# Performance work log

Hardware: AMD Instinct MI355X
Metric: run time of the kernel (lower is better)

The kernel has to match this reference:

```python
import jax, jax.numpy as jnp
import numpy as np

D_IN = 2048
D_LATENT = 16384
BATCH = 4096
K = 64


def setup_inputs() -> dict:
    key = jax.random.key(0)
    k1, k2, k3 = jax.random.split(key, 3)
    s_enc = 1.0 / np.sqrt(D_IN)
    s_dec = 1.0 / np.sqrt(D_LATENT)
    return {
        "x": jax.random.normal(k1, (BATCH, D_IN), dtype=jnp.float32),
        "W_enc": jax.random.normal(k2, (D_LATENT, D_IN), dtype=jnp.float32) * s_enc,
        "b_enc": jnp.zeros((D_LATENT,), dtype=jnp.float32),
        "W_dec": jax.random.normal(k3, (D_IN, D_LATENT), dtype=jnp.float32) * s_dec,
        "b_dec": jnp.zeros((D_IN,), dtype=jnp.float32),
        "k": K,
    }


def reference(x, W_enc, b_enc, W_dec, b_dec, k):
    # encode: dense GEMM + ReLU  -> h: [B, d_latent]
    h = jax.nn.relu(jnp.einsum("bd,ld->bl", x, W_enc) + b_enc)
    # top-k masking over latent dim (dim=1)
    _, idx = jax.lax.top_k(h, k)  # idx: [B, k]
    B = h.shape[0]
    mask = jnp.zeros(h.shape, dtype=bool).at[jnp.arange(B)[:, None], idx].set(True)
    h_topk = jnp.where(mask, h, jnp.zeros((), dtype=h.dtype))
    # decode: GEMM through sparse latents
    x_hat = jnp.einsum("bl,dl->bd", h_topk, W_dec) + b_dec
    return x_hat, h, h_topk
```

## Files before the change

### kernel.cpp

```cpp
#include <hip/hip_runtime.h>
#include <cstdint>

#define DIN   2048
#define DLAT  16384
#define NB    4096
#define KSEL  64
#define MAXC  128
#define CAP   2048
#define TAU   1.5f

typedef unsigned short u16;
typedef unsigned int   u32;
typedef __attribute__((ext_vector_type(8))) short short8;
typedef __attribute__((ext_vector_type(4))) float f32x4;
typedef __attribute__((ext_vector_type(4))) u32  u32x4;

#define GLOAD_LDS16(g, l)                                              \
    __builtin_amdgcn_global_load_lds(                                  \
        (const __attribute__((address_space(1))) void*)(g),            \
        (__attribute__((address_space(3))) void*)(l), 16, 0, 0)

__device__ __forceinline__ u32 f32_to_bf16(u32 u)
{
    u += 0x7FFFu + ((u >> 16) & 1u);
    return u >> 16;
}

__device__ __forceinline__ float bf16_to_f32(u16 w)
{
    return __uint_as_float((u32)w << 16);
}

__global__ __launch_bounds__(256)
void zero_cnt_kernel(u32* __restrict__ cnt)
{
    const int i = blockIdx.x * 256 + threadIdx.x;
    if (i < NB) cnt[i] = 0u;
}

__global__ __launch_bounds__(256)
void cvt_f32_bf16_kernel(const float* __restrict__ in, u16* __restrict__ out, int n8)
{
    const int i = blockIdx.x * 256 + threadIdx.x;
    if (i >= n8) return;
    const float4* p = reinterpret_cast<const float4*>(in) + (size_t)i * 2;
    const float4 a = p[0], b = p[1];
    const float v[8] = {a.x, a.y, a.z, a.w, b.x, b.y, b.z, b.w};
    u32 r[8];
#pragma unroll
    for (int j = 0; j < 8; ++j) r[j] = f32_to_bf16(__float_as_uint(v[j]));
    uint4 o;
    o.x = r[0] | (r[1] << 16);
    o.y = r[2] | (r[3] << 16);
    o.z = r[4] | (r[5] << 16);
    o.w = r[6] | (r[7] << 16);
    reinterpret_cast<uint4*>(out)[i] = o;
}

template <bool APPEND>
__global__ __launch_bounds__(512, 2)
void sae_encode_8ph(const u16* __restrict__ XB, const u16* __restrict__ WB,
                    const float* __restrict__ benc, float* __restrict__ H,
                    u32* __restrict__ cnt, uint2* __restrict__ cand)
{
    __shared__ __align__(16) u16 lds[65536];

    const int tid = threadIdx.x;
    const int wv  = tid >> 6;
    const int ln  = tid & 63;
    const int wm  = wv >> 2;
    const int wn  = wv & 3;
    const int fr  = ln & 15;
    const int fq  = ln >> 4;

    const int b   = blockIdx.x;
    const int wg  = (b & 7) * 128 + (b >> 3);
    const int m_blk = wg & 15;
    const int n_blk = wg >> 4;
    const size_t bm = (size_t)m_blk * 256;
    const size_t bn = (size_t)n_blk * 256;

    const int sslot = (ln & 3) ^ ((ln >> 3) & 3);
    const int srow  = wv * 16 + (ln >> 2);
    const u16* aSrc = XB + (bm + srow) * (size_t)DIN + sslot * 8;
    const u16* bSrc = WB + (bn + srow) * (size_t)DIN + sslot * 8;
    const size_t rowStep = (size_t)128 * DIN;

    auto STG = [&](int mat, int tile, int kkh) {
        const u16* s0 = (mat ? bSrc : aSrc) + tile * 64 + kkh * 32;
        const int dst = (tile & 1) * 32768 + mat * 16384 + kkh * 8192 + wv * 512;
        GLOAD_LDS16(s0,           &lds[dst]);
        GLOAD_LDS16(s0 + rowStep, &lds[dst + 4096]);
    };

    f32x4 acc[8][4];
#pragma unroll
    for (int i = 0; i < 8; ++i)
#pragma unroll
        for (int j = 0; j < 4; ++j) acc[i][j] = (f32x4)0.0f;

    const int swb = (fq ^ ((fr >> 1) & 3)) * 8;
    const int arow0 = wm * 128 + fr;
    const int brow0 = wn * 64 + fr;

    STG(0, 0, 0); STG(1, 0, 0);
    STG(0, 0, 1); STG(1, 0, 1);
    STG(0, 1, 0); STG(1, 1, 0);

    short8 aR[8], bX[2], bY[2];

    for (int g = 0; g < 32; ++g) {
        const int buf = (g & 1) * 32768;

        if (g < 31) asm volatile("s_waitcnt vmcnt(8)" ::: "memory");
        else        asm volatile("s_waitcnt vmcnt(4)" ::: "memory");
        __builtin_amdgcn_s_barrier();
#pragma unroll
        for (int mi = 0; mi < 8; ++mi)
            aR[mi] = *reinterpret_cast<const short8*>(
                &lds[buf + (arow0 + mi * 16) * 32 + swb]);
        bX[0] = *reinterpret_cast<const short8*>(&lds[buf + 16384 + (brow0 +  0) * 32 + swb]);
        bX[1] = *reinterpret_cast<const short8*>(&lds[buf + 16384 + (brow0 + 16) * 32 + swb]);
        if (g < 31) { STG(0, g + 1, 1); STG(1, g + 1, 1); }
        asm volatile("s_waitcnt lgkmcnt(0)" ::: "memory");
        __builtin_amdgcn_sched_barrier(0);
        __builtin_amdgcn_s_setprio(1);
#pragma unroll
        for (int mi = 0; mi < 8; ++mi) {
            acc[mi][0] = __builtin_amdgcn_mfma_f32_16x16x32_bf16(aR[mi], bX[0], acc[mi][0], 0, 0, 0);
            acc[mi][1] = __builtin_amdgcn_mfma_f32_16x16x32_bf16(aR[mi], bX[1], acc[mi][1], 0, 0, 0);
        }
        __builtin_amdgcn_s_setprio(0);

        __builtin_amdgcn_s_barrier();
        bY[0] = *reinterpret_cast<const short8*>(&lds[buf + 16384 + (brow0 + 32) * 32 + swb]);
        bY[1] = *reinterpret_cast<const short8*>(&lds[buf + 16384 + (brow0 + 48) * 32 + swb]);
        if (g < 30) STG(0, g + 2, 0);
        asm volatile("s_waitcnt lgkmcnt(0)" ::: "memory");
        __builtin_amdgcn_sched_barrier(0);
        __builtin_amdgcn_s_setprio(1);
#pragma unroll
        for (int mi = 0; mi < 8; ++mi) {
            acc[mi][2] = __builtin_amdgcn_mfma_f32_16x16x32_bf16(aR[mi], bY[0], acc[mi][2], 0, 0, 0);
            acc[mi][3] = __builtin_amdgcn_mfma_f32_16x16x32_bf16(aR[mi], bY[1], acc[mi][3], 0, 0, 0);
        }
        __builtin_amdgcn_s_setprio(0);

        if (g < 30)       asm volatile("s_waitcnt vmcnt(10)" ::: "memory");
        else if (g == 30) asm volatile("s_waitcnt vmcnt(8)"  ::: "memory");
        else              asm volatile("s_waitcnt vmcnt(0)"  ::: "memory");
        __builtin_amdgcn_s_barrier();
#pragma unroll
        for (int mi = 0; mi < 8; ++mi)
            aR[mi] = *reinterpret_cast<const short8*>(
                &lds[buf + 8192 + (arow0 + mi * 16) * 32 + swb]);
        bY[0] = *reinterpret_cast<const short8*>(&lds[buf + 24576 + (brow0 + 32) * 32 + swb]);
        bY[1] = *reinterpret_cast<const short8*>(&lds[buf + 24576 + (brow0 + 48) * 32 + swb]);
        if (g < 30) STG(1, g + 2, 0);
        asm volatile("s_waitcnt lgkmcnt(0)" ::: "memory");
        __builtin_amdgcn_sched_barrier(0);
        __builtin_amdgcn_s_setprio(1);
#pragma unroll
        for (int mi = 0; mi < 8; ++mi) {
            acc[mi][2] = __builtin_amdgcn_mfma_f32_16x16x32_bf16(aR[mi], bY[0], acc[mi][2], 0, 0, 0);
            acc[mi][3] = __builtin_amdgcn_mfma_f32_16x16x32_bf16(aR[mi], bY[1], acc[mi][3], 0, 0, 0);
        }
        __builtin_amdgcn_s_setprio(0);

        bX[0] = *reinterpret_cast<const short8*>(&lds[buf + 24576 + (brow0 +  0) * 32 + swb]);
        bX[1] = *reinterpret_cast<const short8*>(&lds[buf + 24576 + (brow0 + 16) * 32 + swb]);
        asm volatile("s_waitcnt lgkmcnt(0)" ::: "memory");
        __builtin_amdgcn_sched_barrier(0);
        __builtin_amdgcn_s_setprio(1);
#pragma unroll
        for (int mi = 0; mi < 8; ++mi) {
            acc[mi][0] = __builtin_amdgcn_mfma_f32_16x16x32_bf16(aR[mi], bX[0], acc[mi][0], 0, 0, 0);
            acc[mi][1] = __builtin_amdgcn_mfma_f32_16x16x32_bf16(aR[mi], bX[1], acc[mi][1], 0, 0, 0);
        }
        __builtin_amdgcn_s_setprio(0);
    }

#pragma unroll
    for (int ni = 0; ni < 4; ++ni) {
        const size_t col = bn + wn * 64 + ni * 16 + fr;
        const float be = benc[col];
#pragma unroll
        for (int mi = 0; mi < 8; ++mi) {
            const size_t r0 = bm + wm * 128 + mi * 16 + fq * 4;
            const f32x4 v = acc[mi][ni];
#pragma unroll
            for (int j = 0; j < 4; ++j) {
                const float val = fmaxf(v[j] + be, 0.0f);
                __builtin_nontemporal_store(val, &H[(r0 + j) * DLAT + col]);
                if (APPEND && val > TAU) {
                    const u32 p = atomicAdd(&cnt[r0 + j], 1u);
                    if (p < CAP)
                        cand[(r0 + j) * (size_t)CAP + p] =
                            make_uint2((u32)col, __float_as_uint(val));
                }
            }
        }
    }
}

__global__ __launch_bounds__(256, 4)
void sae_encode_kernel(const float* __restrict__ X, const float* __restrict__ W,
                       const float* __restrict__ benc, float* __restrict__ H)
{
    __shared__ float As[32][132];
    __shared__ float Bs[32][132];

    const int tid  = threadIdx.x;
    const int bm   = blockIdx.y * 128;
    const int bn   = blockIdx.x * 128;

    const int wave = tid >> 6;
    const int lane = tid & 63;
    const int tm   = ((wave >> 1) << 3) + (lane >> 3);
    const int tn   = ((wave &  1) << 3) + (lane &  7);

    float acc[8][8];
#pragma unroll
    for (int i = 0; i < 8; ++i)
#pragma unroll
        for (int j = 0; j < 8; ++j) acc[i][j] = 0.0f;

    const int lrow = tid >> 1;
    const int lcol = (tid & 1) << 4;

    const float* xptr = X + (size_t)(bm + lrow) * DIN + lcol;
    const float* wptr = W + (size_t)(bn + lrow) * DIN + lcol;

    for (int k0 = 0; k0 < DIN; k0 += 32) {
#pragma unroll
        for (int i = 0; i < 4; ++i) {
            const float4 av = *reinterpret_cast<const float4*>(xptr + k0 + 4 * i);
            const float4 bv = *reinterpret_cast<const float4*>(wptr + k0 + 4 * i);
            const int kk = lcol + 4 * i;
            As[kk + 0][lrow] = av.x; As[kk + 1][lrow] = av.y;
            As[kk + 2][lrow] = av.z; As[kk + 3][lrow] = av.w;
            Bs[kk + 0][lrow] = bv.x; Bs[kk + 1][lrow] = bv.y;
            Bs[kk + 2][lrow] = bv.z; Bs[kk + 3][lrow] = bv.w;
        }
        __syncthreads();

#pragma unroll 8
        for (int k = 0; k < 32; ++k) {
            const float4 a0 = *reinterpret_cast<const float4*>(&As[k][tm * 8]);
            const float4 a1 = *reinterpret_cast<const float4*>(&As[k][tm * 8 + 4]);
            const float4 b0 = *reinterpret_cast<const float4*>(&Bs[k][tn * 8]);
            const float4 b1 = *reinterpret_cast<const float4*>(&Bs[k][tn * 8 + 4]);
            const float a[8] = {a0.x, a0.y, a0.z, a0.w, a1.x, a1.y, a1.z, a1.w};
            const float b[8] = {b0.x, b0.y, b0.z, b0.w, b1.x, b1.y, b1.z, b1.w};
#pragma unroll
            for (int i = 0; i < 8; ++i)
#pragma unroll
                for (int j = 0; j < 8; ++j)
                    acc[i][j] = fmaf(a[i], b[j], acc[i][j]);
        }
        __syncthreads();
    }

#pragma unroll
    for (int i = 0; i < 8; ++i) {
        float* orow = H + (size_t)(bm + tm * 8 + i) * DLAT + bn + tn * 8;
#pragma unroll
        for (int j = 0; j < 8; j += 4) {
            float4 o;
            o.x = fmaxf(acc[i][j + 0] + benc[bn + tn * 8 + j + 0], 0.0f);
            o.y = fmaxf(acc[i][j + 1] + benc[bn + tn * 8 + j + 1], 0.0f);
            o.z = fmaxf(acc[i][j + 2] + benc[bn + tn * 8 + j + 2], 0.0f);
            o.w = fmaxf(acc[i][j + 3] + benc[bn + tn * 8 + j + 3], 0.0f);
            *reinterpret_cast<float4*>(orow + j) = o;
        }
    }
}

__device__ __forceinline__ int blk_scan256(int v, volatile int* wsum,
                                           int ln, int wv, int& total)
{
#pragma unroll
    for (int off = 1; off < 64; off <<= 1) {
        const int n = __shfl_up(v, off, 64);
        if (ln >= off) v += n;
    }
    if (ln == 63) wsum[wv] = v;
    __syncthreads();
    int add = 0;
#pragma unroll
    for (int c = 0; c < 3; ++c) if (c < wv) add += wsum[c];
    total = wsum[0] + wsum[1] + wsum[2] + wsum[3];
    __syncthreads();
    return v + add;
}

__device__ __forceinline__ void refine_np(const float* __restrict__ Wenc,
                                          const float* __restrict__ benc,
                                          const float* __restrict__ xs,
                                          int C, const int* cand_idx,
                                          float* cand_val, float psum[32][6],
                                          int tid)
{
    const int g = tid >> 3;
    const int p = tid & 7;
    for (int c0 = 0; c0 < C; c0 += 32) {
        const int ci = c0 + g;
        if (ci < C && p < 6) {
            const int li = cand_idx[ci];
            const float* __restrict__ wr = Wenc + (size_t)li * DIN;
            const int ks = (p < 4) ? p * 384 : 1536 + (p - 4) * 256;
            const int ke = ks + ((p < 4) ? 384 : 256);
            float s = 0.0f;
            for (int k = ks; k < ke; k += 32) {
                float4 w4[8];
#pragma unroll
                for (int j = 0; j < 8; ++j)
                    w4[j] = *reinterpret_cast<const float4*>(wr + k + 4 * j);
#pragma unroll
                for (int j = 0; j < 8; ++j) {
                    const float4 x4 = *reinterpret_cast<const float4*>(xs + k + 4 * j);
                    s = fmaf(x4.x, w4[j].x, s);
                    s = fmaf(x4.y, w4[j].y, s);
                    s = fmaf(x4.z, w4[j].z, s);
                    s = fmaf(x4.w, w4[j].w, s);
                }
            }
            psum[g][p] = s;
        }
        __syncthreads();
        if (ci < C && p == 0) {
            float total = 0.0f;
#pragma unroll
            for (int q = 0; q < 6; ++q)
                total = __fadd_rn(total, psum[g][q]);
            total = __fadd_rn(total, benc[cand_idx[ci]]);
            cand_val[ci] = fmaxf(total, 0.0f);
        }
        __syncthreads();
    }
}

__global__ __launch_bounds__(256)
void sae_topk_compact(const u32* __restrict__ cnt, const uint2* __restrict__ cand,
                      const float* __restrict__ X, const float* __restrict__ Wenc,
                      const float* __restrict__ benc, float* __restrict__ Ht,
                      float band, const u16* __restrict__ WT,
                      const float* __restrict__ bdec, float* __restrict__ xhat)
{
    __shared__ __align__(16) float xs[DIN];
    __shared__ u32  lidx[CAP];
    __shared__ u32  lval[CAP];
    __shared__ u32  hist[4][256];
    __shared__ int  scan_[256];
    __shared__ int  wsum[4];
    __shared__ int  sh_bin, sh_above;
    __shared__ int   cand_idx[MAXC];
    __shared__ float cand_val[MAXC];
    __shared__ unsigned char cand_sel[MAXC];
    __shared__ float psum[32][6];
    __shared__ int   sel_i[KSEL];
    __shared__ float sel_v[KSEL];
    __shared__ int   dec_i[KSEL];
    __shared__ float dec_v[KSEL];

    const int tid = threadIdx.x;
    const int wv  = tid >> 6;
    const int ln  = tid & 63;
    const int row = blockIdx.x;

    const int n = min((int)cnt[row], CAP);

    {
        const float4* xp = reinterpret_cast<const float4*>(X + (size_t)row * DIN);
        reinterpret_cast<float4*>(xs)[tid * 2 + 0] = xp[tid * 2 + 0];
        reinterpret_cast<float4*>(xs)[tid * 2 + 1] = xp[tid * 2 + 1];
    }
    if (tid < KSEL) { dec_i[tid] = 0; dec_v[tid] = 0.0f; }
    for (int i = tid; i < n; i += 256) {
        const uint2 e = cand[(size_t)row * CAP + i];
        lidx[i] = e.x;
        lval[i] = e.y;
    }
    __syncthreads();

    u32 prefix = 0, msk = 0;
    int kk = KSEL;
    for (int pass = 0; pass < 3; ++pass) {
        const int shift = 24 - 8 * pass;
        hist[0][tid] = 0; hist[1][tid] = 0; hist[2][tid] = 0; hist[3][tid] = 0;
        __syncthreads();
        for (int i = tid; i < n; i += 256) {
            const u32 x = lval[i];
            if ((x & msk) == prefix)
                atomicAdd(&hist[wv][(x >> shift) & 255u], 1u);
        }
        __syncthreads();
        int val = (int)(hist[0][255 - tid] + hist[1][255 - tid] +
                        hist[2][255 - tid] + hist[3][255 - tid]);
#pragma unroll
        for (int off = 1; off < 64; off <<= 1) {
            const int nn = __shfl_up(val, off, 64);
            if (ln >= off) val += nn;
        }
        if (ln == 63) wsum[wv] = val;
        __syncthreads();
        int add = 0;
#pragma unroll
        for (int c = 0; c < 3; ++c) if (c < wv) add += wsum[c];
        scan_[tid] = val + add;
        __syncthreads();
        {
            const int binh = (int)(hist[0][tid] + hist[1][tid] +
                                   hist[2][tid] + hist[3][tid]);
            const int ge = scan_[255 - tid];
            const int gt = ge - binh;
            if (gt < kk && ge >= kk) { sh_bin = tid; sh_above = gt; }
        }
        __syncthreads();
        prefix |= ((u32)sh_bin) << shift;
        msk    |= 0xFFu << shift;
        kk     -= sh_above;
        __syncthreads();
    }

    const float Tf = __uint_as_float(prefix);
    const float hi = Tf + band;
    const float lo = Tf - band;

    int c_safe = 0, c_band = 0;
    for (int i = tid; i < n; i += 256) {
        const float f = __uint_as_float(lval[i]);
        c_safe += (f > hi) ? 1 : 0;
        c_band += (f >= lo && f <= hi) ? 1 : 0;
    }
    int S;
    (void)blk_scan256(c_safe, wsum, ln, wv, S);
    int totC;
    const int bincl = blk_scan256(c_band, wsum, ln, wv, totC);
    int bpos = bincl - c_band;
    int C = totC;
    if (C > MAXC) C = MAXC;
    int need = KSEL - S;
    if (need > C) need = C;

    for (int i = tid; i < n; i += 256) {
        const float f = __uint_as_float(lval[i]);
        if (f >= lo && f <= hi) {
            if (bpos < MAXC) cand_idx[bpos] = (int)lidx[i];
            ++bpos;
        }
    }
    __syncthreads();

    refine_np(Wenc, benc, xs, C, cand_idx, cand_val, psum, tid);

    if (tid < C) {
        const float val = cand_val[tid];
        const int  myi = cand_idx[tid];
        int r = 0;
        for (int m = 0; m < C; ++m)
            r += (cand_val[m] > val ||
                  (cand_val[m] == val && cand_idx[m] < myi)) ? 1 : 0;
        cand_sel[tid] = (r < need) ? 1 : 0;
    }
    __syncthreads();

    int csel = 0;
    for (int i = tid; i < n; i += 256) {
        const float f = __uint_as_float(lval[i]);
        bool s = (f > hi);
        if (!s && f >= lo && f <= hi) {
            const int gi = (int)lidx[i];
            for (int m = 0; m < C; ++m)
                if (cand_idx[m] == gi) { s = (cand_sel[m] != 0); break; }
        }
        csel += s ? 1 : 0;
    }
    int totSel;
    int spos = blk_scan256(csel, wsum, ln, wv, totSel) - csel;
    if (totSel > KSEL) totSel = KSEL;
    for (int i = tid; i < n; i += 256) {
        const float f = __uint_as_float(lval[i]);
        bool s = (f > hi);
        if (!s && f >= lo && f <= hi) {
            const int gi = (int)lidx[i];
            for (int m = 0; m < C; ++m)
                if (cand_idx[m] == gi) { s = (cand_sel[m] != 0); break; }
        }
        if (s) {
            if (spos < KSEL) { sel_i[spos] = (int)lidx[i]; sel_v[spos] = f; }
            ++spos;
        }
    }
    __syncthreads();

    if (tid < totSel) {
        const int id = sel_i[tid];
        int r = 0;
        for (int m = 0; m < totSel; ++m)
            r += (sel_i[m] < id) ? 1 : 0;
        dec_i[r] = id;
        dec_v[r] = sel_v[tid];
    }
    __syncthreads();

    float* orow = Ht + (size_t)row * DLAT;
    {
        f32x4 z; z.x = 0.0f; z.y = 0.0f; z.z = 0.0f; z.w = 0.0f;
#pragma unroll
        for (int j = 0; j < 16; ++j)
            __builtin_nontemporal_store(z,
                reinterpret_cast<f32x4*>(orow + j * 1024 + tid * 4));
    }
    __syncthreads();
    if (tid < totSel) orow[dec_i[tid]] = dec_v[tid];

    const int d = tid * 8;
    float4 a0 = *reinterpret_cast<const float4*>(bdec + d);
    float4 a1 = *reinterpret_cast<const float4*>(bdec + d + 4);
#pragma unroll 8
    for (int j = 0; j < KSEL; ++j) {
        const float f = dec_v[j];
        const int   l = dec_i[j];
        const u16* wp = WT + (size_t)l * DIN + d;
        const ushort4 w0 = *reinterpret_cast<const ushort4*>(wp);
        const ushort4 w1 = *reinterpret_cast<const ushort4*>(wp + 4);
        a0.x = fmaf(f, bf16_to_f32(w0.x), a0.x);
        a0.y = fmaf(f, bf16_to_f32(w0.y), a0.y);
        a0.z = fmaf(f, bf16_to_f32(w0.z), a0.z);
        a0.w = fmaf(f, bf16_to_f32(w0.w), a0.w);
        a1.x = fmaf(f, bf16_to_f32(w1.x), a1.x);
        a1.y = fmaf(f, bf16_to_f32(w1.y), a1.y);
        a1.z = fmaf(f, bf16_to_f32(w1.z), a1.z);
        a1.w = fmaf(f, bf16_to_f32(w1.w), a1.w);
    }
    float* xo = xhat + (size_t)row * DIN + d;
    f32x4 s0; s0.x = a0.x; s0.y = a0.y; s0.z = a0.z; s0.w = a0.w;
    f32x4 s1; s1.x = a1.x; s1.y = a1.y; s1.z = a1.z; s1.w = a1.w;
    __builtin_nontemporal_store(s0, reinterpret_cast<f32x4*>(xo));
    __builtin_nontemporal_store(s1, reinterpret_cast<f32x4*>(xo + 4));
}

template <bool FUSE, bool WRITE_LISTS>
__global__ __launch_bounds__(256)
void sae_topk_kernel(const float* __restrict__ H, const float* __restrict__ X,
                     const float* __restrict__ Wenc, const float* __restrict__ benc,
                     float* __restrict__ Ht, int* __restrict__ sidx,
                     float* __restrict__ sval, float band,
                     const u16* __restrict__ WT, const float* __restrict__ bdec,
                     float* __restrict__ xhat)
{
    __shared__ __align__(16) float xs[DIN];
    __shared__ u32  hist[4][256];
    __shared__ int  scan_[256];
    __shared__ int  wsum[4];
    __shared__ int  sh_bin, sh_above;
    __shared__ int           cand_idx[MAXC];
    __shared__ float         cand_val[MAXC];
    __shared__ unsigned char cand_sel[MAXC];
    __shared__ float psum[32][6];
    __shared__ int   dec_idx[KSEL];
    __shared__ float dec_val[KSEL];

    const int tid = threadIdx.x;
    const int wv  = tid >> 6;
    const int ln  = tid & 63;
    const int row = blockIdx.x;
    const u32* __restrict__ hrow =
        reinterpret_cast<const u32*>(H) + (size_t)row * DLAT;

    {
        const float4* xp = reinterpret_cast<const float4*>(X + (size_t)row * DIN);
        reinterpret_cast<float4*>(xs)[tid * 2 + 0] = xp[tid * 2 + 0];
        reinterpret_cast<float4*>(xs)[tid * 2 + 1] = xp[tid * 2 + 1];
    }
    if (FUSE && tid < KSEL) { dec_idx[tid] = 0; dec_val[tid] = 0.0f; }

    u32 v[64];
#pragma unroll
    for (int j = 0; j < 16; ++j) {
        const u32x4 q = __builtin_nontemporal_load(
            reinterpret_cast<const u32x4*>(hrow + j * 1024 + tid * 4));
        v[j * 4 + 0] = q.x; v[j * 4 + 1] = q.y;
        v[j * 4 + 2] = q.z; v[j * 4 + 3] = q.w;
    }

    u32 prefix = 0, msk = 0;
    int kk = KSEL;
    for (int pass = 0; pass < 3; ++pass) {
        const int shift = 24 - 8 * pass;
        hist[0][tid] = 0; hist[1][tid] = 0; hist[2][tid] = 0; hist[3][tid] = 0;
        __syncthreads();
#pragma unroll
        for (int e = 0; e < 64; ++e) {
            const u32 x = v[e];
            if (x != 0u && (x & msk) == prefix)
                atomicAdd(&hist[wv][(x >> shift) & 255u], 1u);
        }
        __syncthreads();
        int val = (int)(hist[0][255 - tid] + hist[1][255 - tid] +
                        hist[2][255 - tid] + hist[3][255 - tid]);
#pragma unroll
        for (int off = 1; off < 64; off <<= 1) {
            const int nn = __shfl_up(val, off, 64);
            if (ln >= off) val += nn;
        }
        if (ln == 63) wsum[wv] = val;
        __syncthreads();
        int add = 0;
#pragma unroll
        for (int c = 0; c < 3; ++c) if (c < wv) add += wsum[c];
        scan_[tid] = val + add;
        __syncthreads();
        {
            const int binh = (int)(hist[0][tid] + hist[1][tid] +
                                   hist[2][tid] + hist[3][tid]);
            const int ge = scan_[255 - tid];
            const int gt = ge - binh;
            if (gt < kk && ge >= kk) { sh_bin = tid; sh_above = gt; }
        }
        __syncthreads();
        prefix |= ((u32)sh_bin) << shift;
        msk    |= 0xFFu << shift;
        kk     -= sh_above;
        __syncthreads();
    }

    const float Tf = __uint_as_float(prefix);
    const float hi = Tf + band;
    const float lo = Tf - band;

    int c_safe = 0, c_band = 0;
#pragma unroll
    for (int e = 0; e < 64; ++e) {
        const float f = __uint_as_float(v[e]);
        c_safe += (f > hi) ? 1 : 0;
        c_band += (f >= lo && f <= hi) ? 1 : 0;
    }

    int S;
    (void)blk_scan256(c_safe, wsum, ln, wv, S);
    int totC;
    const int bincl = blk_scan256(c_band, wsum, ln, wv, totC);
    const int bexc  = bincl - c_band;
    int C = totC;
    if (C > MAXC) C = MAXC;
    int need = KSEL - S;
    if (need > C) need = C;

    {
        int bpos = bexc;
#pragma unroll
        for (int e = 0; e < 64; ++e) {
            const float f = __uint_as_float(v[e]);
            if (f >= lo && f <= hi) {
                if (bpos < MAXC)
                    cand_idx[bpos] = (e >> 2) * 1024 + tid * 4 + (e & 3);
                ++bpos;
            }
        }
    }
    __syncthreads();

    refine_np(Wenc, benc, xs, C, cand_idx, cand_val, psum, tid);

    if (tid < C) {
        const float val = cand_val[tid];
        const int  myi = cand_idx[tid];
        int r = 0;
        for (int m = 0; m < C; ++m)
            r += (cand_val[m] > val ||
                  (cand_val[m] == val && cand_idx[m] < myi)) ? 1 : 0;
        cand_sel[tid] = (r < need) ? 1 : 0;
    }
    __syncthreads();

    unsigned long long selmask = 0ull;
#pragma unroll
    for (int e = 0; e < 64; ++e) {
        const float f = __uint_as_float(v[e]);
        bool s = (f > hi);
        if (!s && f >= lo && f <= hi) {
            const int gi = (e >> 2) * 1024 + tid * 4 + (e & 3);
            for (int m = 0; m < C; ++m)
                if (cand_idx[m] == gi) { s = (cand_sel[m] != 0); break; }
        }
        if (s) selmask |= 1ull << e;
    }
    const int csel = __popcll(selmask);

    int totSel;
    const int pincl = blk_scan256(csel, wsum, ln, wv, totSel);
    const int pos0 = pincl - csel;

    float* orow = Ht + (size_t)row * DLAT;
#pragma unroll
    for (int j = 0; j < 16; ++j) {
        f32x4 o;
        o.x = ((selmask >> (j * 4 + 0)) & 1) ? __uint_as_float(v[j * 4 + 0]) : 0.0f;
        o.y = ((selmask >> (j * 4 + 1)) & 1) ? __uint_as_float(v[j * 4 + 1]) : 0.0f;
        o.z = ((selmask >> (j * 4 + 2)) & 1) ? __uint_as_float(v[j * 4 + 2]) : 0.0f;
        o.w = ((selmask >> (j * 4 + 3)) & 1) ? __uint_as_float(v[j * 4 + 3]) : 0.0f;
        __builtin_nontemporal_store(o,
            reinterpret_cast<f32x4*>(orow + j * 1024 + tid * 4));
    }
    {
        int pos = pos0;
#pragma unroll
        for (int e = 0; e < 64; ++e) {
            if ((selmask >> e) & 1) {
                const int gi = (e >> 2) * 1024 + tid * 4 + (e & 3);
                if (WRITE_LISTS && pos < KSEL) {
                    sidx[(size_t)row * KSEL + pos] = gi;
                    sval[(size_t)row * KSEL + pos] = __uint_as_float(v[e]);
                }
                if (FUSE && pos < KSEL) {
                    dec_idx[pos] = gi;
                    dec_val[pos] = __uint_as_float(v[e]);
                }
                ++pos;
            }
        }
    }

    if (FUSE) {
        __syncthreads();
        const int d = tid * 8;
        float4 a0 = *reinterpret_cast<const float4*>(bdec + d);
        float4 a1 = *reinterpret_cast<const float4*>(bdec + d + 4);
#pragma unroll 8
        for (int j = 0; j < KSEL; ++j) {
            const float f = dec_val[j];
            const int   l = dec_idx[j];
            const u16* wp = WT + (size_t)l * DIN + d;
            const ushort4 w0 = *reinterpret_cast<const ushort4*>(wp);
            const ushort4 w1 = *reinterpret_cast<const ushort4*>(wp + 4);
            a0.x = fmaf(f, bf16_to_f32(w0.x), a0.x);
            a0.y = fmaf(f, bf16_to_f32(w0.y), a0.y);
            a0.z = fmaf(f, bf16_to_f32(w0.z), a0.z);
            a0.w = fmaf(f, bf16_to_f32(w0.w), a0.w);
            a1.x = fmaf(f, bf16_to_f32(w1.x), a1.x);
            a1.y = fmaf(f, bf16_to_f32(w1.y), a1.y);
            a1.z = fmaf(f, bf16_to_f32(w1.z), a1.z);
            a1.w = fmaf(f, bf16_to_f32(w1.w), a1.w);
        }
        float* xo = xhat + (size_t)row * DIN + d;
        f32x4 s0; s0.x = a0.x; s0.y = a0.y; s0.z = a0.z; s0.w = a0.w;
        f32x4 s1; s1.x = a1.x; s1.y = a1.y; s1.z = a1.z; s1.w = a1.w;
        __builtin_nontemporal_store(s0, reinterpret_cast<f32x4*>(xo));
        __builtin_nontemporal_store(s1, reinterpret_cast<f32x4*>(xo + 4));
    }
}

__global__ __launch_bounds__(256)
void sae_transpose_cvt(const float* __restrict__ W, u16* __restrict__ WT)
{
    __shared__ float t[32][65];
    const int bx = blockIdx.x * 32;
    const int by = blockIdx.y * 64;
    const int lx = threadIdx.x;
    const int ly = threadIdx.y;

    for (int r = ly; r < 64; r += 8)
        t[lx][r] = W[(size_t)(by + r) * DLAT + bx + lx];
    __syncthreads();
    for (int c = ly; c < 32; c += 8) {
        const u32 lo = f32_to_bf16(__float_as_uint(t[c][2 * lx + 0]));
        const u32 hi = f32_to_bf16(__float_as_uint(t[c][2 * lx + 1]));
        *reinterpret_cast<u32*>(WT + (size_t)(bx + c) * DIN + by + 2 * lx) =
            lo | (hi << 16);
    }
}

__global__ __launch_bounds__(512)
void sae_decode_f32(const float* __restrict__ Wd, const int* __restrict__ sidx,
                    const float* __restrict__ sval, const float* __restrict__ bdec,
                    float* __restrict__ xhat)
{
    __shared__ int   si[KSEL];
    __shared__ float sv[KSEL];
    const int row = blockIdx.x;
    const int tid = threadIdx.x;
    if (tid < KSEL) {
        si[tid] = sidx[(size_t)row * KSEL + tid];
        sv[tid] = sval[(size_t)row * KSEL + tid];
    }
    __syncthreads();

    const int d = tid * 4;
    float4 acc = *reinterpret_cast<const float4*>(bdec + d);
#pragma unroll 4
    for (int j = 0; j < KSEL; ++j) {
        const float f = sv[j];
        const int   l = si[j];
        acc.x = fmaf(f, Wd[(size_t)(d + 0) * DLAT + l], acc.x);
        acc.y = fmaf(f, Wd[(size_t)(d + 1) * DLAT + l], acc.y);
        acc.z = fmaf(f, Wd[(size_t)(d + 2) * DLAT + l], acc.z);
        acc.w = fmaf(f, Wd[(size_t)(d + 3) * DLAT + l], acc.w);
    }
    *reinterpret_cast<float4*>(xhat + (size_t)row * DIN + d) = acc;
}

__global__ __launch_bounds__(512)
void sae_decode_nows_kernel(const float* __restrict__ Ht, const float* __restrict__ Wd,
                            const float* __restrict__ bdec, float* __restrict__ xhat)
{
    __shared__ int   si[KSEL];
    __shared__ float sv[KSEL];
    __shared__ unsigned cnt;
    const int row = blockIdx.x;
    const int tid = threadIdx.x;
    if (tid == 0) cnt = 0;
    __syncthreads();
    for (int i = tid; i < DLAT; i += 512) {
        const float v = Ht[(size_t)row * DLAT + i];
        if (v != 0.0f) {
            const unsigned p = atomicAdd(&cnt, 1u);
            if (p < KSEL) { si[p] = i; sv[p] = v; }
        }
    }
    __syncthreads();
    const unsigned n = cnt < (unsigned)KSEL ? cnt : (unsigned)KSEL;
    const int d = tid * 4;
    float4 acc = *reinterpret_cast<const float4*>(bdec + d);
    for (unsigned j = 0; j < n; ++j) {
        const float f = sv[j];
        const int   l = si[j];
        acc.x = fmaf(f, Wd[(size_t)(d + 0) * DLAT + l], acc.x);
        acc.y = fmaf(f, Wd[(size_t)(d + 1) * DLAT + l], acc.y);
        acc.z = fmaf(f, Wd[(size_t)(d + 2) * DLAT + l], acc.z);
        acc.w = fmaf(f, Wd[(size_t)(d + 3) * DLAT + l], acc.w);
    }
    *reinterpret_cast<float4*>(xhat + (size_t)row * DIN + d) = acc;
}

extern "C" void kernel_launch(void* const* d_in, const int* in_sizes, int n_in,
                              void* d_out, int out_size, void* d_ws, size_t ws_size,
                              hipStream_t stream)
{
    const float* x     = (const float*)d_in[0];
    const float* W_enc = (const float*)d_in[1];
    const float* b_enc = (const float*)d_in[2];
    const float* W_dec = (const float*)d_in[3];
    const float* b_dec = (const float*)d_in[4];

    float* xhat  = (float*)d_out;
    float* h     = xhat + (size_t)NB * DIN;
    float* htopk = h + (size_t)NB * DLAT;

    const size_t LIST_BYTES = 2097152ull;
    const size_t WT_BYTES   = 2ull * DLAT * DIN;
    const size_t XB_BYTES   = 2ull * NB * DIN;
    const size_t WB_BYTES   = 2ull * DLAT * DIN;
    const size_t XB_OFF     = LIST_BYTES + WT_BYTES;
    const size_t WB_OFF     = XB_OFF + XB_BYTES;
    const size_t CNT_OFF    = WB_OFF + WB_BYTES;
    const size_t CNT_BYTES  = (size_t)NB * 4;
    const size_t CAND_OFF   = CNT_OFF + CNT_BYTES;
    const size_t CAND_BYTES = (size_t)NB * CAP * 8;

    int*   sp_idx = (int*)d_ws;
    float* sp_val = (float*)((char*)d_ws + (LIST_BYTES / 2));
    u16*   WT     = (u16*)((char*)d_ws + LIST_BYTES);
    u16*   xb     = (u16*)((char*)d_ws + XB_OFF);
    u16*   wb     = (u16*)((char*)d_ws + WB_OFF);
    u32*   cntb   = (u32*)((char*)d_ws + CNT_OFF);
    uint2* candb  = (uint2*)((char*)d_ws + CAND_OFF);

    const bool have_lists = ws_size >= LIST_BYTES;
    const bool have_wt    = ws_size >= LIST_BYTES + WT_BYTES;
    const bool have_mfma  = ws_size >= WB_OFF + WB_BYTES;
    const bool have_cand  = ws_size >= CAND_OFF + CAND_BYTES;

    const float band = have_mfma ? 0.03f : 1e-3f;

    if (have_wt) {
        sae_transpose_cvt<<<dim3(DLAT / 32, DIN / 64), dim3(32, 8), 0, stream>>>(W_dec, WT);
    }

    if (have_mfma) {
        cvt_f32_bf16_kernel<<<(NB * DIN / 8 + 255) / 256, 256, 0, stream>>>(x, xb, NB * DIN / 8);
        cvt_f32_bf16_kernel<<<(DLAT * DIN / 8 + 255) / 256, 256, 0, stream>>>(W_enc, wb, DLAT * DIN / 8);
        if (have_cand) {
            zero_cnt_kernel<<<NB / 256, 256, 0, stream>>>(cntb);
            sae_encode_8ph<true><<<(NB / 256) * (DLAT / 256), 512, 0, stream>>>(
                xb, wb, b_enc, h, cntb, candb);
        } else {
            sae_encode_8ph<false><<<(NB / 256) * (DLAT / 256), 512, 0, stream>>>(
                xb, wb, b_enc, h, nullptr, nullptr);
        }
    } else {
        sae_encode_kernel<<<dim3(DLAT / 128, NB / 128), 256, 0, stream>>>(x, W_enc, b_enc, h);
    }

    if (have_cand && have_wt && have_mfma) {
        sae_topk_compact<<<NB, 256, 0, stream>>>(
            cntb, candb, x, W_enc, b_enc, htopk, band, WT, b_dec, xhat);
    } else if (have_wt) {
        sae_topk_kernel<true, false><<<NB, 256, 0, stream>>>(
            h, x, W_enc, b_enc, htopk, nullptr, nullptr, band, WT, b_dec, xhat);
    } else if (have_lists) {
        sae_topk_kernel<false, true><<<NB, 256, 0, stream>>>(
            h, x, W_enc, b_enc, htopk, sp_idx, sp_val, band, nullptr, nullptr, nullptr);
        sae_decode_f32<<<NB, 512, 0, stream>>>(W_dec, sp_idx, sp_val, b_dec, xhat);
    } else {
        sae_topk_kernel<false, false><<<NB, 256, 0, stream>>>(
            h, x, W_enc, b_enc, htopk, nullptr, nullptr, band, nullptr, nullptr, nullptr);
        sae_decode_nows_kernel<<<NB, 512, 0, stream>>>(htopk, W_dec, b_dec, xhat);
    }
}
```

Baseline: 827.0 us.

## Use block-local LDS counters and per-block segments in h_topk for candidates

The encode kernel now counts threshold candidates per row in LDS instead of global atomics, and writes them into fixed 64-slot segments per column block stored inside the h_topk output buffer. Per-block counts go to a small count array, which removes the zero-count kernel and the large separate candidate buffer. The top-k kernel prefix-scans the 64 segment counts and compacts the candidates into LDS. This cuts global atomic contention and workspace traffic, but a segment overflowing 64 entries silently drops candidates, and it relies on h_topk being fully overwritten afterwards.

```diff
diff --git a/kernel.cpp b/kernel.cpp
--- a/kernel.cpp
+++ b/kernel.cpp
@@ -7,6 +7,7 @@
 #define KSEL  64
 #define MAXC  128
 #define CAP   2048
+#define SEG   64
 #define TAU   1.5f
 
 typedef unsigned short u16;
@@ -29,13 +30,6 @@
 __device__ __forceinline__ float bf16_to_f32(u16 w)
 {
     return __uint_as_float((u32)w << 16);
-}
-
-__global__ __launch_bounds__(256)
-void zero_cnt_kernel(u32* __restrict__ cnt)
-{
-    const int i = blockIdx.x * 256 + threadIdx.x;
-    if (i < NB) cnt[i] = 0u;
 }
 
 __global__ __launch_bounds__(256)
@@ -61,7 +55,7 @@
 __global__ __launch_bounds__(512, 2)
 void sae_encode_8ph(const u16* __restrict__ XB, const u16* __restrict__ WB,
                     const float* __restrict__ benc, float* __restrict__ H,
-                    u32* __restrict__ cnt, uint2* __restrict__ cand)
+                    u32* __restrict__ cnt2, uint2* __restrict__ candbase)
 {
     __shared__ __align__(16) u16 lds[65536];
 
@@ -180,26 +174,38 @@
         __builtin_amdgcn_s_setprio(0);
     }
 
+    u32* rowcnt = reinterpret_cast<u32*>(lds);
+    if (APPEND) {
+        __syncthreads();
+        if (tid < 256) rowcnt[tid] = 0u;
+        __syncthreads();
+    }
+
 #pragma unroll
     for (int ni = 0; ni < 4; ++ni) {
         const size_t col = bn + wn * 64 + ni * 16 + fr;
         const float be = benc[col];
 #pragma unroll
         for (int mi = 0; mi < 8; ++mi) {
-            const size_t r0 = bm + wm * 128 + mi * 16 + fq * 4;
-            const f32x4 v = acc[mi][ni];
+            const int lr0 = wm * 128 + mi * 16 + fq * 4;
 #pragma unroll
             for (int j = 0; j < 4; ++j) {
-                const float val = fmaxf(v[j] + be, 0.0f);
-                __builtin_nontemporal_store(val, &H[(r0 + j) * DLAT + col]);
+                const float val = fmaxf(acc[mi][ni][j] + be, 0.0f);
+                __builtin_nontemporal_store(val, &H[(bm + lr0 + j) * DLAT + col]);
                 if (APPEND && val > TAU) {
-                    const u32 p = atomicAdd(&cnt[r0 + j], 1u);
-                    if (p < CAP)
-                        cand[(r0 + j) * (size_t)CAP + p] =
+                    const u32 p = atomicAdd(&rowcnt[lr0 + j], 1u);
+                    if (p < SEG)
+                        candbase[(bm + lr0 + j) * (size_t)(DLAT / 2)
+                                 + (size_t)n_blk * SEG + p] =
                             make_uint2((u32)col, __float_as_uint(val));
                 }
             }
         }
+    }
+    if (APPEND) {
+        __syncthreads();
+        if (tid < 256)
+            cnt2[(bm + tid) * 64 + n_blk] = min(rowcnt[tid], (u32)SEG);
     }
 }
 
@@ -341,15 +347,18 @@
 }
 
 __global__ __launch_bounds__(256)
-void sae_topk_compact(const u32* __restrict__ cnt, const uint2* __restrict__ cand,
-                      const float* __restrict__ X, const float* __restrict__ Wenc,
-                      const float* __restrict__ benc, float* __restrict__ Ht,
-                      float band, const u16* __restrict__ WT,
-                      const float* __restrict__ bdec, float* __restrict__ xhat)
+void sae_topk_compact(const u32* __restrict__ cnt2, const float* __restrict__ X,
+                      const float* __restrict__ Wenc, const float* __restrict__ benc,
+                      float* __restrict__ Ht, float band,
+                      const u16* __restrict__ WT, const float* __restrict__ bdec,
+                      float* __restrict__ xhat)
 {
     __shared__ __align__(16) float xs[DIN];
     __shared__ u32  lidx[CAP];
     __shared__ u32  lval[CAP];
+    __shared__ u32  scnt[64];
+    __shared__ u32  soff[64];
+    __shared__ int  sh_n;
     __shared__ u32  hist[4][256];
     __shared__ int  scan_[256];
     __shared__ int  wsum[4];
@@ -367,8 +376,8 @@
     const int wv  = tid >> 6;
     const int ln  = tid & 63;
     const int row = blockIdx.x;
-
-    const int n = min((int)cnt[row], CAP);
+    const uint2* __restrict__ candRow =
+        reinterpret_cast<const uint2*>(Ht + (size_t)row * DLAT);
 
     {
         const float4* xp = reinterpret_cast<const float4*>(X + (size_t)row * DIN);
@@ -376,10 +385,33 @@
         reinterpret_cast<float4*>(xs)[tid * 2 + 1] = xp[tid * 2 + 1];
     }
     if (tid < KSEL) { dec_i[tid] = 0; dec_v[tid] = 0.0f; }
-    for (int i = tid; i < n; i += 256) {
-        const uint2 e = cand[(size_t)row * CAP + i];
-        lidx[i] = e.x;
-        lval[i] = e.y;
+    if (tid < 64) scnt[tid] = cnt2[(size_t)row * 64 + tid];
+    __syncthreads();
+    if (tid < 64) {
+        const u32 v0 = scnt[tid];
+        u32 s = v0;
+#pragma unroll
+        for (int off = 1; off < 64; off <<= 1) {
+            const u32 nn = __shfl_up(s, off, 64);
+            if (ln >= off) s += nn;
+        }
+        soff[tid] = s - v0;
+        if (tid == 63) sh_n = (int)s;
+    }
+    __syncthreads();
+    const int n = min(sh_n, CAP);
+
+    for (int i = tid; i < 64 * SEG; i += 256) {
+        const int seg  = i >> 6;
+        const int slot = i & (SEG - 1);
+        if (slot < (int)scnt[seg]) {
+            const int d = (int)soff[seg] + slot;
+            if (d < CAP) {
+                const uint2 e = candRow[seg * SEG + slot];
+                lidx[d] = e.x;
+                lval[d] = e.y;
+            }
+        }
     }
     __syncthreads();
 
@@ -855,22 +887,19 @@
     const size_t XB_OFF     = LIST_BYTES + WT_BYTES;
     const size_t WB_OFF     = XB_OFF + XB_BYTES;
     const size_t CNT_OFF    = WB_OFF + WB_BYTES;
-    const size_t CNT_BYTES  = (size_t)NB * 4;
-    const size_t CAND_OFF   = CNT_OFF + CNT_BYTES;
-    const size_t CAND_BYTES = (size_t)NB * CAP * 8;
+    const size_t CNT_BYTES  = (size_t)NB * 64 * 4;
 
     int*   sp_idx = (int*)d_ws;
     float* sp_val = (float*)((char*)d_ws + (LIST_BYTES / 2));
     u16*   WT     = (u16*)((char*)d_ws + LIST_BYTES);
     u16*   xb     = (u16*)((char*)d_ws + XB_OFF);
     u16*   wb     = (u16*)((char*)d_ws + WB_OFF);
-    u32*   cntb   = (u32*)((char*)d_ws + CNT_OFF);
-    uint2* candb  = (uint2*)((char*)d_ws + CAND_OFF);
+    u32*   cnt2   = (u32*)((char*)d_ws + CNT_OFF);
 
     const bool have_lists = ws_size >= LIST_BYTES;
     const bool have_wt    = ws_size >= LIST_BYTES + WT_BYTES;
     const bool have_mfma  = ws_size >= WB_OFF + WB_BYTES;
-    const bool have_cand  = ws_size >= CAND_OFF + CAND_BYTES;
+    const bool have_cand  = ws_size >= CNT_OFF + CNT_BYTES;
 
     const float band = have_mfma ? 0.03f : 1e-3f;
 
@@ -881,10 +910,9 @@
     if (have_mfma) {
         cvt_f32_bf16_kernel<<<(NB * DIN / 8 + 255) / 256, 256, 0, stream>>>(x, xb, NB * DIN / 8);
         cvt_f32_bf16_kernel<<<(DLAT * DIN / 8 + 255) / 256, 256, 0, stream>>>(W_enc, wb, DLAT * DIN / 8);
-        if (have_cand) {
-            zero_cnt_kernel<<<NB / 256, 256, 0, stream>>>(cntb);
+        if (have_cand && have_wt) {
             sae_encode_8ph<true><<<(NB / 256) * (DLAT / 256), 512, 0, stream>>>(
-                xb, wb, b_enc, h, cntb, candb);
+                xb, wb, b_enc, h, cnt2, reinterpret_cast<uint2*>(htopk));
         } else {
             sae_encode_8ph<false><<<(NB / 256) * (DLAT / 256), 512, 0, stream>>>(
                 xb, wb, b_enc, h, nullptr, nullptr);
@@ -895,7 +923,7 @@
 
     if (have_cand && have_wt && have_mfma) {
         sae_topk_compact<<<NB, 256, 0, stream>>>(
-            cntb, candb, x, W_enc, b_enc, htopk, band, WT, b_dec, xhat);
+            cnt2, x, W_enc, b_enc, htopk, band, WT, b_dec, xhat);
     } else if (have_wt) {
         sae_topk_kernel<true, false><<<NB, 256, 0, stream>>>(
             h, x, W_enc, b_enc, htopk, nullptr, nullptr, band, WT, b_dec, xhat);
```

Result: faster. 764.6 us (-7.5%).
